# Kernel tuning notes

Hardware: AMD Instinct MI355X
Metric: run time of the kernel (lower is better)

Reference implementation:

```python
import jax, jax.numpy as jnp
import numpy as np

HIDDEN = 1024
NUM_HEADS = 16
GROUP_SIZE = 2
GROUP_NUM = NUM_HEADS // GROUP_SIZE
HEAD_DIM = HIDDEN // NUM_HEADS


def setup_inputs() -> dict:
    key = jax.random.key(0)
    ks = jax.random.split(key, 9)
    B, S = 1, 4096
    s = 0.02
    return {
        "hidden_state": jax.random.normal(ks[0], (B, S, HIDDEN), jnp.float32),
        "Wq": jax.random.normal(ks[1], (HIDDEN, HIDDEN), jnp.float32) * s,
        "bq": jnp.zeros((HIDDEN,), jnp.float32),
        "Wk": jax.random.normal(ks[2], (HIDDEN, GROUP_NUM * HEAD_DIM), jnp.float32) * s,
        "bk": jnp.zeros((GROUP_NUM * HEAD_DIM,), jnp.float32),
        "Wv": jax.random.normal(ks[3], (HIDDEN, GROUP_NUM * HEAD_DIM), jnp.float32) * s,
        "bv": jnp.zeros((GROUP_NUM * HEAD_DIM,), jnp.float32),
        "Wo": jax.random.normal(ks[4], (HIDDEN, HIDDEN), jnp.float32) * s,
        "bo": jnp.zeros((HIDDEN,), jnp.float32),
    }


def reference(hidden_state, Wq, bq, Wk, bk, Wv, bv, Wo, bo):
    B, S, _ = hidden_state.shape
    # projections
    q = hidden_state @ Wq + bq                      # [B,S,H*hd]
    k = hidden_state @ Wk + bk                      # [B,S,G*hd]
    v = hidden_state @ Wv + bv                      # [B,S,G*hd]
    q = q.reshape(B, S, NUM_HEADS, HEAD_DIM).transpose(0, 2, 1, 3)   # [B,H,S,hd]
    k = k.reshape(B, S, GROUP_NUM, HEAD_DIM).transpose(0, 2, 1, 3)   # [B,G,S,hd]
    v = v.reshape(B, S, GROUP_NUM, HEAD_DIM).transpose(0, 2, 1, 3)
    # expand KV heads: each kv head repeated group_size times consecutively
    k = jnp.repeat(k, GROUP_SIZE, axis=1)           # [B,H,S,hd]
    v = jnp.repeat(v, GROUP_SIZE, axis=1)
    scale = 1.0 / np.sqrt(HEAD_DIM).astype(np.float32)
    scores = jnp.einsum('bhqd,bhkd->bhqk', q, k) * scale   # [B,H,S,S]
    attn = jax.nn.softmax(scores, axis=-1)
    ctx = jnp.einsum('bhqk,bhkd->bhqd', attn, v)    # [B,H,S,hd]
    ctx = ctx.transpose(0, 2, 1, 3).reshape(B, S, HIDDEN)
    return ctx @ Wo + bo
```

## Files before the change

### kernel.cpp

```cpp
#include <hip/hip_runtime.h>
#include <hip/hip_bf16.h>
#include <cstdint>
#include <cstddef>

typedef __bf16 bf16x8 __attribute__((ext_vector_type(8)));
typedef float f32x4 __attribute__((ext_vector_type(4)));
typedef float f32x16 __attribute__((ext_vector_type(16)));
typedef uint32_t u32x4 __attribute__((ext_vector_type(4)));
typedef __hip_bfloat16 bf16h;

__device__ __forceinline__ unsigned short bf16bits(float f) {
  bf16h h = __float2bfloat16(f);
  return __builtin_bit_cast(unsigned short, h);
}
__device__ __forceinline__ float bf16tof(unsigned short u) {
  union { uint32_t i; float f; } v; v.i = (uint32_t)u << 16; return v.f;
}

__global__ void cast_f32_bf16(const float* __restrict__ src, bf16h* __restrict__ dst, int n) {
  int i = (blockIdx.x * blockDim.x + threadIdx.x) * 4;
  if (i >= n) return;
  float4 v = *reinterpret_cast<const float4*>(src + i);
  ushort4 o;
  o.x = bf16bits(v.x); o.y = bf16bits(v.y); o.z = bf16bits(v.z); o.w = bf16bits(v.w);
  *reinterpret_cast<ushort4*>(dst + i) = o;
}

__global__ __launch_bounds__(256) void prep_weights(const float* __restrict__ Wq, const float* __restrict__ Wk,
                                                    const float* __restrict__ Wv, const float* __restrict__ Wo,
                                                    const float* __restrict__ bq, const float* __restrict__ bk,
                                                    const float* __restrict__ bv,
                                                    bf16h* __restrict__ WcT, bf16h* __restrict__ WoT,
                                                    float* __restrict__ bcat, float qscale) {
  int b = blockIdx.x;
  int tx = threadIdx.x, ty = threadIdx.y;
  if (b >= 3072) {
    int i = (b - 3072) * 256 + ty * 32 + tx;
    bcat[i] = (i < 1024) ? bq[i] * qscale : (i < 1536 ? bk[i - 1024] : bv[i - 1536]);
    return;
  }
  const float* src; bf16h* dst; int C, bx, by; float sc = 1.0f;
  if (b < 1024)      { src = Wq; dst = WcT;               C = 1024; bx = b & 31;          by = b >> 5; sc = qscale; }
  else if (b < 1536) { src = Wk; dst = WcT + 1024 * 1024; C = 512;  bx = (b - 1024) & 15; by = (b - 1024) >> 4; }
  else if (b < 2048) { src = Wv; dst = WcT + 1536 * 1024; C = 512;  bx = (b - 1536) & 15; by = (b - 1536) >> 4; }
  else               { src = Wo; dst = WoT;               C = 1024; bx = (b - 2048) & 31; by = (b - 2048) >> 5; }
  __shared__ float tile[32][33];
  int c0 = bx * 32, r0 = by * 32;
  #pragma unroll
  for (int i = 0; i < 32; i += 8)
    tile[ty + i][tx] = src[(size_t)(r0 + ty + i) * C + c0 + tx];
  __syncthreads();
  #pragma unroll
  for (int i = 0; i < 32; i += 8)
    dst[(size_t)(c0 + ty + i) * 1024 + r0 + tx] = __float2bfloat16(tile[tx][ty + i] * sc);
}

__global__ __launch_bounds__(256) void gemm_qkv(const bf16h* __restrict__ A, const bf16h* __restrict__ BT,
                                                const float* __restrict__ bias,
                                                bf16h* __restrict__ qb, bf16h* __restrict__ kperm,
                                                bf16h* __restrict__ vperm) {
  __shared__ __align__(16) bf16h As[128 * 64];
  __shared__ __align__(16) bf16h Bs[128 * 64];
  const int tid = threadIdx.x;
  const int lane = tid & 63;
  const int m0 = blockIdx.y * 128, n0 = blockIdx.x * 128;
  const int wid = tid >> 6, wr = wid >> 1, wc = wid & 1;
  const int cl = lane & 15, rg = lane >> 4;
  const int srow = tid >> 3, scol = (tid & 7) * 8;
  const int K = 1024;
  f32x4 acc[4][4] = {};

  for (int k0 = 0; k0 < K; k0 += 64) {
    __syncthreads();
    #pragma unroll
    for (int i = 0; i < 4; ++i) {
      int r = i * 32 + srow;
      __builtin_amdgcn_global_load_lds(
          (__attribute__((address_space(1))) void*)(A + (size_t)(m0 + r) * K + k0 + scol),
          (__attribute__((address_space(3))) void*)(As + i * 2048 + tid * 8), 16, 0, 0);
    }
    #pragma unroll
    for (int i = 0; i < 4; ++i) {
      int r = i * 32 + srow;
      __builtin_amdgcn_global_load_lds(
          (__attribute__((address_space(1))) void*)(BT + (size_t)(n0 + r) * K + k0 + scol),
          (__attribute__((address_space(3))) void*)(Bs + i * 2048 + tid * 8), 16, 0, 0);
    }
    __syncthreads();
    #pragma unroll
    for (int ks = 0; ks < 2; ++ks) {
      bf16x8 af[4], bfr[4];
      #pragma unroll
      for (int mi = 0; mi < 4; ++mi)
        af[mi] = *reinterpret_cast<const bf16x8*>(As + (wr * 64 + mi * 16 + cl) * 64 + ks * 32 + rg * 8);
      #pragma unroll
      for (int ni = 0; ni < 4; ++ni)
        bfr[ni] = *reinterpret_cast<const bf16x8*>(Bs + (wc * 64 + ni * 16 + cl) * 64 + ks * 32 + rg * 8);
      #pragma unroll
      for (int mi = 0; mi < 4; ++mi)
        #pragma unroll
        for (int ni = 0; ni < 4; ++ni)
          acc[mi][ni] = __builtin_amdgcn_mfma_f32_16x16x32_bf16(af[mi], bfr[ni], acc[mi][ni], 0, 0, 0);
    }
  }

  if (n0 < 1024) {
    #pragma unroll
    for (int ni = 0; ni < 4; ++ni) {
      int col = n0 + wc * 64 + ni * 16 + cl;
      float bv = bias[col];
      #pragma unroll
      for (int mi = 0; mi < 4; ++mi)
        #pragma unroll
        for (int j = 0; j < 4; ++j) {
          int row = m0 + wr * 64 + mi * 16 + rg * 4 + j;
          qb[(size_t)row * 1024 + col] = __float2bfloat16(acc[mi][ni][j] + bv);
        }
    }
  } else if (n0 < 1536) {
    #pragma unroll
    for (int ni = 0; ni < 4; ++ni) {
      int col = n0 + wc * 64 + ni * 16 + cl;
      float bv = bias[col];
      int cd = col - 1024, gg = cd >> 6, d = cd & 63;
      int ds = d >> 4, hh = (d >> 3) & 1, e = d & 7;
      size_t cbase = (size_t)gg * 262144 + (size_t)ds * 512 + hh * 256 + e;
      #pragma unroll
      for (int mi = 0; mi < 4; ++mi) {
        int row0 = m0 + wr * 64 + mi * 16 + rg * 4;
        #pragma unroll
        for (int j = 0; j < 4; ++j) {
          int k = row0 + j;
          kperm[cbase + (size_t)(k >> 5) * 2048 + (k & 31) * 8] = __float2bfloat16(acc[mi][ni][j] + bv);
        }
      }
    }
  } else {
    #pragma unroll
    for (int ni = 0; ni < 4; ++ni) {
      int col = n0 + wc * 64 + ni * 16 + cl;
      float bv = bias[col];
      int cd = col - 1536, gg = cd >> 6, d = cd & 63;
      int l31 = d & 31, dh = d >> 5;
      #pragma unroll
      for (int mi = 0; mi < 4; ++mi) {
        int row0 = m0 + wr * 64 + mi * 16 + rg * 4;
        int kt = row0 >> 5, ks = (row0 >> 4) & 1, hh = (row0 >> 3) & 1, e0 = row0 & 7;
        ushort4 o;
        o.x = bf16bits(acc[mi][ni][0] + bv);
        o.y = bf16bits(acc[mi][ni][1] + bv);
        o.z = bf16bits(acc[mi][ni][2] + bv);
        o.w = bf16bits(acc[mi][ni][3] + bv);
        *reinterpret_cast<ushort4*>(vperm + ((size_t)gg * 128 + kt) * 2048 +
                                    (size_t)(ks * 2 + dh) * 512 + (hh * 32 + l31) * 8 + e0) = o;
      }
    }
  }
}

template <typename OutT>
__global__ __launch_bounds__(256) void gemm_bt(const bf16h* __restrict__ A, const bf16h* __restrict__ BT,
                                               const float* __restrict__ bias, OutT* __restrict__ C,
                                               int M, int N, int K) {
  __shared__ __align__(16) bf16h As[128 * 64];
  __shared__ __align__(16) bf16h Bs[128 * 64];
  const int tid = threadIdx.x;
  const int lane = tid & 63;
  const int m0 = blockIdx.y * 128, n0 = blockIdx.x * 128;
  const int wid = tid >> 6, wr = wid >> 1, wc = wid & 1;
  const int cl = lane & 15, rg = lane >> 4;
  const int srow = tid >> 3, scol = (tid & 7) * 8;
  f32x4 acc[4][4] = {};

  for (int k0 = 0; k0 < K; k0 += 64) {
    __syncthreads();
    #pragma unroll
    for (int i = 0; i < 4; ++i) {
      int r = i * 32 + srow;
      __builtin_amdgcn_global_load_lds(
          (__attribute__((address_space(1))) void*)(A + (size_t)(m0 + r) * K + k0 + scol),
          (__attribute__((address_space(3))) void*)(As + i * 2048 + tid * 8), 16, 0, 0);
    }
    #pragma unroll
    for (int i = 0; i < 4; ++i) {
      int r = i * 32 + srow;
      __builtin_amdgcn_global_load_lds(
          (__attribute__((address_space(1))) void*)(BT + (size_t)(n0 + r) * K + k0 + scol),
          (__attribute__((address_space(3))) void*)(Bs + i * 2048 + tid * 8), 16, 0, 0);
    }
    __syncthreads();
    #pragma unroll
    for (int ks = 0; ks < 2; ++ks) {
      bf16x8 af[4], bfr[4];
      #pragma unroll
      for (int mi = 0; mi < 4; ++mi)
        af[mi] = *reinterpret_cast<const bf16x8*>(As + (wr * 64 + mi * 16 + cl) * 64 + ks * 32 + rg * 8);
      #pragma unroll
      for (int ni = 0; ni < 4; ++ni)
        bfr[ni] = *reinterpret_cast<const bf16x8*>(Bs + (wc * 64 + ni * 16 + cl) * 64 + ks * 32 + rg * 8);
      #pragma unroll
      for (int mi = 0; mi < 4; ++mi)
        #pragma unroll
        for (int ni = 0; ni < 4; ++ni)
          acc[mi][ni] = __builtin_amdgcn_mfma_f32_16x16x32_bf16(af[mi], bfr[ni], acc[mi][ni], 0, 0, 0);
    }
  }
  #pragma unroll
  for (int ni = 0; ni < 4; ++ni) {
    int col = n0 + wc * 64 + ni * 16 + cl;
    float bv = bias[col];
    #pragma unroll
    for (int mi = 0; mi < 4; ++mi)
      #pragma unroll
      for (int j = 0; j < 4; ++j) {
        int row = m0 + wr * 64 + mi * 16 + rg * 4 + j;
        C[(size_t)row * N + col] = acc[mi][ni][j] + bv;
      }
  }
}

__global__ __launch_bounds__(64, 2) void attn_fwd(const bf16h* __restrict__ qb,
                                                  const bf16h* __restrict__ kperm,
                                                  const bf16h* __restrict__ vperm,
                                                  bf16h* __restrict__ part,
                                                  float* __restrict__ lpart) {
  const int tid = threadIdx.x, l31 = tid & 31, hi = tid >> 5;
  const int bid = blockIdx.x;
  const int g = bid & 7;
  const int r2 = bid >> 3;
  const int qx = r2 & 63, hl = (r2 >> 6) & 1, c = r2 >> 7;
  const int h = g * 2 + hl;
  const int q0 = qx * 64;
  const int kt0 = c * 64;

  bf16x8 qfA[4], qfB[4];
  {
    const bf16h* qrA = qb + (size_t)(q0 + l31) * 1024 + h * 64 + hi * 8;
    #pragma unroll
    for (int ds = 0; ds < 4; ++ds) {
      qfA[ds] = *reinterpret_cast<const bf16x8*>(qrA + ds * 16);
      qfB[ds] = *reinterpret_cast<const bf16x8*>(qrA + (size_t)32 * 1024 + ds * 16);
    }
  }

  const bf16h* kg = kperm + ((size_t)g << 18) + tid * 8;
  const bf16h* vg = vperm + ((size_t)g << 18) + tid * 8;

  f32x16 oA0, oA1, oB0, oB1;
  #pragma unroll
  for (int i = 0; i < 16; ++i) { oA0[i] = 0.f; oA1[i] = 0.f; oB0[i] = 0.f; oB1[i] = 0.f; }
  float lsA = 0.f, lsB = 0.f;

  auto LOAD = [&](bf16x8 (&Kf)[4], bf16x8 (&Vf)[4], int kt) {
    const bf16h* kb = kg + (size_t)kt * 2048;
    const bf16h* vb = vg + (size_t)kt * 2048;
    #pragma unroll
    for (int s = 0; s < 4; ++s) {
      Kf[s] = *reinterpret_cast<const bf16x8*>(kb + s * 512);
      Vf[s] = *reinterpret_cast<const bf16x8*>(vb + s * 512);
    }
  };

  auto build_pa = [&](const f32x16& S, int u) -> bf16x8 {
    uint32_t w0, w1, w2, w3;
    asm("v_cvt_pk_bf16_f32 %0, %1, %2" : "=v"(w0) : "v"(S[8 * u + 0]), "v"(S[8 * u + 1]));
    asm("v_cvt_pk_bf16_f32 %0, %1, %2" : "=v"(w1) : "v"(S[8 * u + 2]), "v"(S[8 * u + 3]));
    asm("v_cvt_pk_bf16_f32 %0, %1, %2" : "=v"(w2) : "v"(S[8 * u + 4]), "v"(S[8 * u + 5]));
    asm("v_cvt_pk_bf16_f32 %0, %1, %2" : "=v"(w3) : "v"(S[8 * u + 6]), "v"(S[8 * u + 7]));
    asm("v_permlane32_swap_b32 %0, %1" : "+v"(w0), "+v"(w2));
    asm("v_permlane32_swap_b32 %0, %1" : "+v"(w1), "+v"(w3));
    u32x4 pw; pw[0] = w0; pw[1] = w1; pw[2] = w2; pw[3] = w3;
    return __builtin_bit_cast(bf16x8, pw);
  };

  auto BODY = [&](const bf16x8 (&Kf)[4], const bf16x8 (&Vf)[4]) {
    f32x16 sA, sB;
    #pragma unroll
    for (int i = 0; i < 16; ++i) { sA[i] = 0.f; sB[i] = 0.f; }
    __builtin_amdgcn_s_setprio(1);
    #pragma unroll
    for (int ds = 0; ds < 4; ++ds) {
      sA = __builtin_amdgcn_mfma_f32_32x32x16_bf16(Kf[ds], qfA[ds], sA, 0, 0, 0);
      sB = __builtin_amdgcn_mfma_f32_32x32x16_bf16(Kf[ds], qfB[ds], sB, 0, 0, 0);
    }
    __builtin_amdgcn_s_setprio(0);
    float ra0 = 0.f, ra1 = 0.f, rb0 = 0.f, rb1 = 0.f;
    #pragma unroll
    for (int r = 0; r < 16; r += 4) {
      #pragma unroll
      for (int j = 0; j < 4; ++j) {
        sA[r + j] = __builtin_amdgcn_exp2f(sA[r + j]);
        sB[r + j] = __builtin_amdgcn_exp2f(sB[r + j]);
      }
      ra0 += sA[r] + sA[r + 1]; ra1 += sA[r + 2] + sA[r + 3];
      rb0 += sB[r] + sB[r + 1]; rb1 += sB[r + 2] + sB[r + 3];
    }
    float rsA = ra0 + ra1, rsB = rb0 + rb1;
    lsA += rsA + __shfl_xor(rsA, 32);
    lsB += rsB + __shfl_xor(rsB, 32);
    __builtin_amdgcn_s_setprio(1);
    #pragma unroll
    for (int u = 0; u < 2; ++u) {
      bf16x8 paA = build_pa(sA, u);
      bf16x8 paB = build_pa(sB, u);
      oA0 = __builtin_amdgcn_mfma_f32_32x32x16_bf16(Vf[u * 2 + 0], paA, oA0, 0, 0, 0);
      oA1 = __builtin_amdgcn_mfma_f32_32x32x16_bf16(Vf[u * 2 + 1], paA, oA1, 0, 0, 0);
      oB0 = __builtin_amdgcn_mfma_f32_32x32x16_bf16(Vf[u * 2 + 0], paB, oB0, 0, 0, 0);
      oB1 = __builtin_amdgcn_mfma_f32_32x32x16_bf16(Vf[u * 2 + 1], paB, oB1, 0, 0, 0);
    }
    __builtin_amdgcn_s_setprio(0);
  };

  bf16x8 Ka[4], Va[4], Kb[4], Vb[4];
  LOAD(Ka, Va, kt0);
  for (int tt = 0; tt < 64; tt += 2) {
    int t1 = kt0 + tt + 1; if (t1 > 127) t1 = 127;
    LOAD(Kb, Vb, t1);
    BODY(Ka, Va);
    int t2 = kt0 + tt + 2; if (t2 > 127) t2 = 127;
    LOAD(Ka, Va, t2);
    BODY(Kb, Vb);
  }

  {
    int qA = q0 + l31, qB = qA + 32;
    bf16h* pA = part + ((size_t)(c * 4096 + qA) * 16 + h) * 64;
    bf16h* pB = part + ((size_t)(c * 4096 + qB) * 16 + h) * 64;
    #pragma unroll
    for (int dh = 0; dh < 2; ++dh) {
      const f32x16& aA = dh ? oA1 : oA0;
      const f32x16& aB = dh ? oB1 : oB0;
      #pragma unroll
      for (int t = 0; t < 4; ++t) {
        int d0 = dh * 32 + 8 * t + 4 * hi;
        ushort4 sa, sb;
        sa.x = bf16bits(aA[4 * t + 0]); sa.y = bf16bits(aA[4 * t + 1]);
        sa.z = bf16bits(aA[4 * t + 2]); sa.w = bf16bits(aA[4 * t + 3]);
        sb.x = bf16bits(aB[4 * t + 0]); sb.y = bf16bits(aB[4 * t + 1]);
        sb.z = bf16bits(aB[4 * t + 2]); sb.w = bf16bits(aB[4 * t + 3]);
        *reinterpret_cast<ushort4*>(pA + d0) = sa;
        *reinterpret_cast<ushort4*>(pB + d0) = sb;
      }
    }
    if (hi == 0) {
      lpart[(size_t)(c * 4096 + qA) * 16 + h] = lsA;
      lpart[(size_t)(c * 4096 + qB) * 16 + h] = lsB;
    }
  }
}

__global__ __launch_bounds__(256) void combine_part(const bf16h* __restrict__ part,
                                                    const float* __restrict__ lpart,
                                                    bf16h* __restrict__ ctx) {
  int idx = blockIdx.x * 256 + threadIdx.x;
  int q = idx >> 4, h = idx & 15;
  const bf16h* p0 = part + ((size_t)q * 16 + h) * 64;
  const bf16h* p1 = p0 + (size_t)4096 * 1024;
  float inv = 1.0f / (lpart[(size_t)q * 16 + h] + lpart[(size_t)4096 * 16 + q * 16 + h]);
  bf16h* o = ctx + (size_t)q * 1024 + h * 64;
  #pragma unroll
  for (int w = 0; w < 8; ++w) {
    ushort4 a = *reinterpret_cast<const ushort4*>(p0 + w * 8);
    ushort4 b = *reinterpret_cast<const ushort4*>(p1 + w * 8);
    ushort4 c2 = *reinterpret_cast<const ushort4*>(p0 + w * 8 + 4);
    ushort4 d2 = *reinterpret_cast<const ushort4*>(p1 + w * 8 + 4);
    ushort4 r0, r1;
    r0.x = bf16bits((bf16tof(a.x) + bf16tof(b.x)) * inv);
    r0.y = bf16bits((bf16tof(a.y) + bf16tof(b.y)) * inv);
    r0.z = bf16bits((bf16tof(a.z) + bf16tof(b.z)) * inv);
    r0.w = bf16bits((bf16tof(a.w) + bf16tof(b.w)) * inv);
    r1.x = bf16bits((bf16tof(c2.x) + bf16tof(d2.x)) * inv);
    r1.y = bf16bits((bf16tof(c2.y) + bf16tof(d2.y)) * inv);
    r1.z = bf16bits((bf16tof(c2.z) + bf16tof(d2.z)) * inv);
    r1.w = bf16bits((bf16tof(c2.w) + bf16tof(d2.w)) * inv);
    *reinterpret_cast<ushort4*>(o + w * 8) = r0;
    *reinterpret_cast<ushort4*>(o + w * 8 + 4) = r1;
  }
}

extern "C" void kernel_launch(void* const* d_in, const int* in_sizes, int n_in,
                              void* d_out, int out_size, void* d_ws, size_t ws_size,
                              hipStream_t stream) {
  const float* hs = (const float*)d_in[0];
  const float* Wq = (const float*)d_in[1];
  const float* bq = (const float*)d_in[2];
  const float* Wk = (const float*)d_in[3];
  const float* bk = (const float*)d_in[4];
  const float* Wv = (const float*)d_in[5];
  const float* bv = (const float*)d_in[6];
  const float* Wo = (const float*)d_in[7];
  const float* bo = (const float*)d_in[8];
  float* out = (float*)d_out;

  const float QSCALE = 0.125f * 1.44269504088896f;

  char* ws = (char*)d_ws;
  const size_t MB = 1u << 20;
  bf16h* hb    = (bf16h*)(ws);
  bf16h* WcT   = (bf16h*)(ws + 8 * MB);
  bf16h* part  = (bf16h*)(ws);
  float* lpart = (float*)(ws + 16 * MB);
  bf16h* qb    = (bf16h*)(ws + 17 * MB);
  bf16h* ctx   = (bf16h*)(ws + 17 * MB);
  bf16h* kperm = (bf16h*)(ws + 25 * MB);
  bf16h* vperm = (bf16h*)(ws + 29 * MB);
  bf16h* WoT   = (bf16h*)(ws + 33 * MB);
  float* bcat  = (float*)(ws + 35 * MB);

  cast_f32_bf16<<<dim3(4096), dim3(256), 0, stream>>>(hs, hb, 4096 * 1024);
  prep_weights<<<dim3(3080), dim3(32, 8), 0, stream>>>(Wq, Wk, Wv, Wo, bq, bk, bv,
                                                       WcT, WoT, bcat, QSCALE);
  gemm_qkv<<<dim3(16, 32), dim3(256), 0, stream>>>(hb, WcT, bcat, qb, kperm, vperm);
  attn_fwd<<<dim3(2048), dim3(64), 0, stream>>>(qb, kperm, vperm, part, lpart);
  combine_part<<<dim3(256), dim3(256), 0, stream>>>(part, lpart, ctx);
  gemm_bt<float><<<dim3(8, 32), dim3(256), 0, stream>>>(ctx, WoT, bo, out, 4096, 1024, 1024);
}
```

Baseline: 149.4 us.

## Split KV across four waves per block and merge partials in shared memory

```diff
diff --git a/kernel.cpp b/kernel.cpp
--- a/kernel.cpp
+++ b/kernel.cpp
@@ -12,9 +12,6 @@
 __device__ __forceinline__ unsigned short bf16bits(float f) {
   bf16h h = __float2bfloat16(f);
   return __builtin_bit_cast(unsigned short, h);
-}
-__device__ __forceinline__ float bf16tof(unsigned short u) {
-  union { uint32_t i; float f; } v; v.i = (uint32_t)u << 16; return v.f;
 }
 
 __global__ void cast_f32_bf16(const float* __restrict__ src, bf16h* __restrict__ dst, int n) {
@@ -158,9 +155,8 @@
   }
 }
 
-template <typename OutT>
 __global__ __launch_bounds__(256) void gemm_bt(const bf16h* __restrict__ A, const bf16h* __restrict__ BT,
-                                               const float* __restrict__ bias, OutT* __restrict__ C,
+                                               const float* __restrict__ bias, float* __restrict__ C,
                                                int M, int N, int K) {
   __shared__ __align__(16) bf16h As[128 * 64];
   __shared__ __align__(16) bf16h Bs[128 * 64];
@@ -219,19 +215,20 @@
   }
 }
 
-__global__ __launch_bounds__(64, 2) void attn_fwd(const bf16h* __restrict__ qb,
-                                                  const bf16h* __restrict__ kperm,
-                                                  const bf16h* __restrict__ vperm,
-                                                  bf16h* __restrict__ part,
-                                                  float* __restrict__ lpart) {
-  const int tid = threadIdx.x, l31 = tid & 31, hi = tid >> 5;
+__global__ __launch_bounds__(256, 2) void attn_fwd(const bf16h* __restrict__ qb,
+                                                   const bf16h* __restrict__ kperm,
+                                                   const bf16h* __restrict__ vperm,
+                                                   bf16h* __restrict__ ctx) {
+  __shared__ float oL[4][64][33];
+  __shared__ float lsL[4][64];
+  const int t256 = threadIdx.x;
+  const int wid = t256 >> 6, lane = t256 & 63;
+  const int l31 = lane & 31, hi = lane >> 5;
   const int bid = blockIdx.x;
-  const int g = bid & 7;
-  const int r2 = bid >> 3;
-  const int qx = r2 & 63, hl = (r2 >> 6) & 1, c = r2 >> 7;
+  const int g = bid & 7, hl = (bid >> 3) & 1, qx = bid >> 4;
   const int h = g * 2 + hl;
   const int q0 = qx * 64;
-  const int kt0 = c * 64;
+  const int kt0 = wid * 32;
 
   bf16x8 qfA[4], qfB[4];
   {
@@ -243,8 +240,8 @@
     }
   }
 
-  const bf16h* kg = kperm + ((size_t)g << 18) + tid * 8;
-  const bf16h* vg = vperm + ((size_t)g << 18) + tid * 8;
+  const bf16h* kg = kperm + ((size_t)g << 18) + lane * 8;
+  const bf16h* vg = vperm + ((size_t)g << 18) + lane * 8;
 
   f32x16 oA0, oA1, oB0, oB1;
   #pragma unroll
@@ -313,69 +310,43 @@
 
   bf16x8 Ka[4], Va[4], Kb[4], Vb[4];
   LOAD(Ka, Va, kt0);
-  for (int tt = 0; tt < 64; tt += 2) {
-    int t1 = kt0 + tt + 1; if (t1 > 127) t1 = 127;
-    LOAD(Kb, Vb, t1);
+  for (int tt = 0; tt < 32; tt += 2) {
+    LOAD(Kb, Vb, kt0 + tt + 1);
     BODY(Ka, Va);
-    int t2 = kt0 + tt + 2; if (t2 > 127) t2 = 127;
+    int t2 = (tt + 2 <= 31) ? kt0 + tt + 2 : kt0 + 31;
     LOAD(Ka, Va, t2);
     BODY(Kb, Vb);
   }
 
-  {
-    int qA = q0 + l31, qB = qA + 32;
-    bf16h* pA = part + ((size_t)(c * 4096 + qA) * 16 + h) * 64;
-    bf16h* pB = part + ((size_t)(c * 4096 + qB) * 16 + h) * 64;
-    #pragma unroll
-    for (int dh = 0; dh < 2; ++dh) {
-      const f32x16& aA = dh ? oA1 : oA0;
-      const f32x16& aB = dh ? oB1 : oB0;
-      #pragma unroll
-      for (int t = 0; t < 4; ++t) {
-        int d0 = dh * 32 + 8 * t + 4 * hi;
-        ushort4 sa, sb;
-        sa.x = bf16bits(aA[4 * t + 0]); sa.y = bf16bits(aA[4 * t + 1]);
-        sa.z = bf16bits(aA[4 * t + 2]); sa.w = bf16bits(aA[4 * t + 3]);
-        sb.x = bf16bits(aB[4 * t + 0]); sb.y = bf16bits(aB[4 * t + 1]);
-        sb.z = bf16bits(aB[4 * t + 2]); sb.w = bf16bits(aB[4 * t + 3]);
-        *reinterpret_cast<ushort4*>(pA + d0) = sa;
-        *reinterpret_cast<ushort4*>(pB + d0) = sb;
-      }
-    }
-    if (hi == 0) {
-      lpart[(size_t)(c * 4096 + qA) * 16 + h] = lsA;
-      lpart[(size_t)(c * 4096 + qB) * 16 + h] = lsB;
-    }
-  }
-}
-
-__global__ __launch_bounds__(256) void combine_part(const bf16h* __restrict__ part,
-                                                    const float* __restrict__ lpart,
-                                                    bf16h* __restrict__ ctx) {
-  int idx = blockIdx.x * 256 + threadIdx.x;
-  int q = idx >> 4, h = idx & 15;
-  const bf16h* p0 = part + ((size_t)q * 16 + h) * 64;
-  const bf16h* p1 = p0 + (size_t)4096 * 1024;
-  float inv = 1.0f / (lpart[(size_t)q * 16 + h] + lpart[(size_t)4096 * 16 + q * 16 + h]);
-  bf16h* o = ctx + (size_t)q * 1024 + h * 64;
-  #pragma unroll
-  for (int w = 0; w < 8; ++w) {
-    ushort4 a = *reinterpret_cast<const ushort4*>(p0 + w * 8);
-    ushort4 b = *reinterpret_cast<const ushort4*>(p1 + w * 8);
-    ushort4 c2 = *reinterpret_cast<const ushort4*>(p0 + w * 8 + 4);
-    ushort4 d2 = *reinterpret_cast<const ushort4*>(p1 + w * 8 + 4);
-    ushort4 r0, r1;
-    r0.x = bf16bits((bf16tof(a.x) + bf16tof(b.x)) * inv);
-    r0.y = bf16bits((bf16tof(a.y) + bf16tof(b.y)) * inv);
-    r0.z = bf16bits((bf16tof(a.z) + bf16tof(b.z)) * inv);
-    r0.w = bf16bits((bf16tof(a.w) + bf16tof(b.w)) * inv);
-    r1.x = bf16bits((bf16tof(c2.x) + bf16tof(d2.x)) * inv);
-    r1.y = bf16bits((bf16tof(c2.y) + bf16tof(d2.y)) * inv);
-    r1.z = bf16bits((bf16tof(c2.z) + bf16tof(d2.z)) * inv);
-    r1.w = bf16bits((bf16tof(c2.w) + bf16tof(d2.w)) * inv);
-    *reinterpret_cast<ushort4*>(o + w * 8) = r0;
-    *reinterpret_cast<ushort4*>(o + w * 8 + 4) = r1;
-  }
+  auto merge_pass = [&](const f32x16& x0, const f32x16& x1, float lsv, int qbase) {
+    #pragma unroll
+    for (int i = 0; i < 16; ++i) {
+      oL[wid][lane][i] = x0[i];
+      oL[wid][lane][16 + i] = x1[i];
+    }
+    lsL[wid][lane] = lsv;
+    __syncthreads();
+    float inv = 1.0f / (lsL[0][lane] + lsL[1][lane] + lsL[2][lane] + lsL[3][lane]);
+    const int r0 = 8 * wid;
+    float m[8];
+    #pragma unroll
+    for (int k = 0; k < 8; ++k)
+      m[k] = (oL[0][lane][r0 + k] + oL[1][lane][r0 + k] +
+              oL[2][lane][r0 + k] + oL[3][lane][r0 + k]) * inv;
+    bf16h* op = ctx + (size_t)(qbase + l31) * 1024 + h * 64;
+    #pragma unroll
+    for (int half = 0; half < 2; ++half) {
+      int r = r0 + half * 4;
+      int d0 = 32 * (r >> 4) + 8 * ((r & 15) >> 2) + 4 * hi;
+      ushort4 st;
+      st.x = bf16bits(m[half * 4 + 0]); st.y = bf16bits(m[half * 4 + 1]);
+      st.z = bf16bits(m[half * 4 + 2]); st.w = bf16bits(m[half * 4 + 3]);
+      *reinterpret_cast<ushort4*>(op + d0) = st;
+    }
+    __syncthreads();
+  };
+  merge_pass(oA0, oA1, lsA, q0);
+  merge_pass(oB0, oB1, lsB, q0 + 32);
 }
 
 extern "C" void kernel_launch(void* const* d_in, const int* in_sizes, int n_in,
@@ -397,21 +368,18 @@
   char* ws = (char*)d_ws;
   const size_t MB = 1u << 20;
   bf16h* hb    = (bf16h*)(ws);
+  bf16h* ctx   = (bf16h*)(ws);
   bf16h* WcT   = (bf16h*)(ws + 8 * MB);
-  bf16h* part  = (bf16h*)(ws);
-  float* lpart = (float*)(ws + 16 * MB);
-  bf16h* qb    = (bf16h*)(ws + 17 * MB);
-  bf16h* ctx   = (bf16h*)(ws + 17 * MB);
-  bf16h* kperm = (bf16h*)(ws + 25 * MB);
-  bf16h* vperm = (bf16h*)(ws + 29 * MB);
-  bf16h* WoT   = (bf16h*)(ws + 33 * MB);
-  float* bcat  = (float*)(ws + 35 * MB);
+  bf16h* qb    = (bf16h*)(ws + 12 * MB);
+  bf16h* kperm = (bf16h*)(ws + 20 * MB);
+  bf16h* vperm = (bf16h*)(ws + 24 * MB);
+  bf16h* WoT   = (bf16h*)(ws + 28 * MB);
+  float* bcat  = (float*)(ws + 30 * MB);
 
   cast_f32_bf16<<<dim3(4096), dim3(256), 0, stream>>>(hs, hb, 4096 * 1024);
   prep_weights<<<dim3(3080), dim3(32, 8), 0, stream>>>(Wq, Wk, Wv, Wo, bq, bk, bv,
                                                        WcT, WoT, bcat, QSCALE);
   gemm_qkv<<<dim3(16, 32), dim3(256), 0, stream>>>(hb, WcT, bcat, qb, kperm, vperm);
-  attn_fwd<<<dim3(2048), dim3(64), 0, stream>>>(qb, kperm, vperm, part, lpart);
-  combine_part<<<dim3(256), dim3(256), 0, stream>>>(part, lpart, ctx);
-  gemm_bt<float><<<dim3(8, 32), dim3(256), 0, stream>>>(ctx, WoT, bo, out, 4096, 1024, 1024);
-}
+  attn_fwd<<<dim3(1024), dim3(256), 0, stream>>>(qb, kperm, vperm, ctx);
+  gemm_bt<<<dim3(8, 32), dim3(256), 0, stream>>>(ctx, WoT, bo, out, 4096, 1024, 1024);
+}
```

Result: faster. 144.7 us (-3.1%).
